# Performance work log

Measured on AMD Instinct MI355X. Metric: run time of the kernel, lower is better.

Reference implementation:

```python
import jax, jax.numpy as jnp
import numpy as np

N_NODES = 50000
N_EDGES = 1600000
F_GO, F_RE, F_ME = 512, 256, 256
E_DIM, N_HEADS, H_DIM, O_DIM = 256, 4, 256, 128


def setup_inputs() -> dict:
    key = jax.random.key(0)
    ks = jax.random.split(key, 20)
    s = lambda k, shp, sc: jax.random.normal(k, shp, dtype=jnp.float32) * sc
    inp = {
        "x": jax.random.normal(ks[0], (N_NODES, F_GO + F_RE + F_ME + 1), dtype=jnp.float32),
        "edge_index": jax.random.randint(ks[1], (2, N_EDGES), 0, N_NODES, dtype=jnp.int32),
        # modality projections (stored as [in, out] so we do x @ W)
        "w_go": s(ks[2], (F_GO, E_DIM), 0.04), "b_go": jnp.zeros((E_DIM,), jnp.float32),
        "w_re": s(ks[3], (F_RE, E_DIM), 0.06), "b_re": jnp.zeros((E_DIM,), jnp.float32),
        "w_me": s(ks[4], (F_ME, E_DIM), 0.06), "b_me": jnp.zeros((E_DIM,), jnp.float32),
        "w_gw": s(ks[5], (1, E_DIM), 0.5),    "b_gw": jnp.zeros((E_DIM,), jnp.float32),
        # MultiheadAttention params (torch layout: in_proj_w [3E, E], out_proj_w [E, E])
        "in_proj_w": s(ks[6], (3 * E_DIM, E_DIM), 0.06),
        "in_proj_b": jnp.zeros((3 * E_DIM,), jnp.float32),
        "out_proj_w": s(ks[7], (E_DIM, E_DIM), 0.06),
        "out_proj_b": jnp.zeros((E_DIM,), jnp.float32),
        # GCN layers (stored as [in, out])
        "w1": s(ks[8], (E_DIM, H_DIM), 0.06), "b1": jnp.zeros((H_DIM,), jnp.float32),
        "w2": s(ks[9], (H_DIM, O_DIM), 0.06), "b2": jnp.zeros((O_DIM,), jnp.float32),
    }
    return inp


def _forward(x, edge_index, w_go, b_go, w_re, b_re, w_me, b_me, w_gw, b_gw,
             in_proj_w, in_proj_b, out_proj_w, out_proj_b, w1, b1, w2, b2):
    N = x.shape[0]
    relu = jax.nn.relu
    go = x[:, :F_GO]
    re_ = x[:, F_GO:F_GO + F_RE]
    me = x[:, F_GO + F_RE:F_GO + F_RE + F_ME]
    gw = x[:, -1:]  # gwas = last column
    # [N, 4, E]: four projected modalities stacked as a tiny sequence
    p = jnp.stack([relu(go @ w_go + b_go), relu(re_ @ w_re + b_re),
                   relu(me @ w_me + b_me), relu(gw @ w_gw + b_gw)], axis=1)
    # Multihead self-attention over the 4 modality tokens
    wq, wk, wv = jnp.split(in_proj_w, 3, axis=0)
    bq, bk, bv = jnp.split(in_proj_b, 3, axis=0)
    dh = E_DIM // N_HEADS
    q = (p @ wq.T + bq).reshape(N, 4, N_HEADS, dh)
    k = (p @ wk.T + bk).reshape(N, 4, N_HEADS, dh)
    v = (p @ wv.T + bv).reshape(N, 4, N_HEADS, dh)
    scores = jnp.einsum('nqhd,nkhd->nhqk', q, k) / jnp.sqrt(jnp.float32(dh))
    attn = jax.nn.softmax(scores, axis=-1)
    o = jnp.einsum('nhqk,nkhd->nqhd', attn, v).reshape(N, 4, E_DIM)
    o = o @ out_proj_w.T + out_proj_b
    fused = o.mean(axis=1)  # [N, E]
    # GCN normalization with self-loops (shared by both layers)
    loops = jnp.arange(N, dtype=edge_index.dtype)
    src = jnp.concatenate([edge_index[0], loops])
    dst = jnp.concatenate([edge_index[1], loops])
    deg = jax.ops.segment_sum(jnp.ones_like(src, dtype=fused.dtype), dst, num_segments=N)
    dinv = jnp.where(deg > 0, jax.lax.rsqrt(deg), 0.0)
    norm = dinv[src] * dinv[dst]  # [E+N]

    def gcn(h, W, b):
        hw = h @ W  # transform then scatter-aggregate
        msg = norm[:, None] * hw[src]
        return jax.ops.segment_sum(msg, dst, num_segments=N) + b

    h1 = relu(gcn(fused, w1, b1))
    # dropout p=0.3 skipped (eval mode)
    return gcn(h1, w2, b2)


def reference(x, edge_index, w_go, b_go, w_re, b_re, w_me, b_me, w_gw, b_gw,
              in_proj_w, in_proj_b, out_proj_w, out_proj_b, w1, b1, w2, b2):
    return _forward(x, edge_index, w_go, b_go, w_re, b_re, w_me, b_me, w_gw, b_gw,
                    in_proj_w, in_proj_b, out_proj_w, out_proj_b, w1, b1, w2, b2)
```

## Files before the change

### kernel.cpp

```cpp
#include <hip/hip_runtime.h>
#include <cstdint>
#include <cstddef>

#define NN 50000
#define NE 1600000
#define XD 1025

typedef unsigned short ushortt;
typedef __attribute__((ext_vector_type(8))) short short8;
typedef __attribute__((ext_vector_type(4))) float f32x4;

__device__ __forceinline__ float relu_f(float v) { return v > 0.f ? v : 0.f; }
__device__ __forceinline__ float b2f(ushortt u) { return __uint_as_float(((unsigned)u) << 16); }
__device__ __forceinline__ float blo(unsigned u) { return __uint_as_float(u << 16); }
__device__ __forceinline__ float bhi(unsigned u) { return __uint_as_float(u & 0xffff0000u); }
__device__ __forceinline__ ushortt bf16rn(float f) {
    unsigned u = __float_as_uint(f);
    return (ushortt)((u + 0x7fffu + ((u >> 16) & 1u)) >> 16);
}
__device__ __forceinline__ void load_lds16(const void* g, void* l) {
    __builtin_amdgcn_global_load_lds(
        (const __attribute__((address_space(1))) void*)g,
        (__attribute__((address_space(3))) void*)l, 16, 0, 0);
}

template <int ACT>
__global__ __launch_bounds__(256) void gemm_mfma(
    const ushortt* __restrict__ A, int lda,
    const ushortt* __restrict__ Bt,
    ushortt* __restrict__ C, int ldc,
    const float* __restrict__ bias,
    int M, int K)
{
    __shared__ ushortt As[128 * 32];
    __shared__ ushortt Bs[128 * 32];
    const int tid = threadIdx.x;
    const int w = tid >> 6, l = tid & 63;
    const int wr = w >> 1, wc = w & 1;
    const int brow = blockIdx.y << 7;
    const int bcol = blockIdx.x << 7;

    f32x4 acc[4][4] = {};

    const int rA0 = wr * 64 + (l & 15);
    const int rB0 = wc * 64 + (l & 15);
    const int kslot = l >> 4;

    for (int k0 = 0; k0 < K; k0 += 32) {
#pragma unroll
        for (int c = 0; c < 2; ++c) {
            int rl = c * 64 + w * 16 + (l >> 2);
            int csel = (l & 3) ^ (rl & 3);
            int gr = brow + rl; if (gr >= M) gr = M - 1;
            load_lds16(A + (size_t)gr * lda + k0 + csel * 8, &As[(c * 64 + w * 16) * 32]);
        }
#pragma unroll
        for (int c = 0; c < 2; ++c) {
            int rl = c * 64 + w * 16 + (l >> 2);
            int csel = (l & 3) ^ (rl & 3);
            load_lds16(Bt + (size_t)(bcol + rl) * K + k0 + csel * 8, &Bs[(c * 64 + w * 16) * 32]);
        }
        __syncthreads();

        short8 af[4], bf[4];
#pragma unroll
        for (int mi = 0; mi < 4; ++mi) {
            int row = rA0 + mi * 16;
            af[mi] = *(const short8*)&As[row * 32 + ((kslot ^ (row & 3)) << 3)];
        }
#pragma unroll
        for (int ni = 0; ni < 4; ++ni) {
            int row = rB0 + ni * 16;
            bf[ni] = *(const short8*)&Bs[row * 32 + ((kslot ^ (row & 3)) << 3)];
        }
#pragma unroll
        for (int mi = 0; mi < 4; ++mi)
#pragma unroll
            for (int ni = 0; ni < 4; ++ni)
                acc[mi][ni] = __builtin_amdgcn_mfma_f32_16x16x32_bf16(af[mi], bf[ni], acc[mi][ni], 0, 0, 0);
        __syncthreads();
    }

    const int cb = bcol + wc * 64 + (l & 15);
    const int rb = brow + wr * 64 + ((l >> 4) << 2);
#pragma unroll
    for (int mi = 0; mi < 4; ++mi) {
#pragma unroll
        for (int ni = 0; ni < 4; ++ni) {
            int col = cb + ni * 16;
            float bv = bias ? bias[col] : 0.f;
#pragma unroll
            for (int r = 0; r < 4; ++r) {
                int row = rb + mi * 16 + r;
                if (row < M) {
                    float v = acc[mi][ni][r] + bv;
                    if (ACT == 1) v = relu_f(v);
                    C[(size_t)row * ldc + col] = bf16rn(v);
                }
            }
        }
    }
}

__global__ __launch_bounds__(256) void mega_a2(
    const float* __restrict__ x,
    const float* __restrict__ w_go, const float* __restrict__ w_re,
    const float* __restrict__ w_me, const float* __restrict__ w2,
    const float* __restrict__ ipw,
    ushortt* __restrict__ o_go, ushortt* __restrict__ o_re,
    ushortt* __restrict__ o_me, ushortt* __restrict__ o_w2, ushortt* __restrict__ o_ip,
    ushortt* __restrict__ ago, ushortt* __restrict__ are, ushortt* __restrict__ ame,
    const float* __restrict__ w_gw, const float* __restrict__ b_gw, ushortt* __restrict__ p,
    const float* __restrict__ opw, const float* __restrict__ w1, float* __restrict__ T)
{
    const int bid = blockIdx.x;
    const int tid = threadIdx.x;
    if (bid < 25000) {
        long idx = bid * 256L + tid;
        int n = (int)(idx >> 7);
        int c8 = ((int)idx & 127) << 3;
        const float* src = x + (size_t)n * XD + c8;
        ushortt* dstp;
        if (c8 < 512) dstp = ago + (size_t)n * 512 + c8;
        else if (c8 < 768) dstp = are + (size_t)n * 256 + (c8 - 512);
        else dstp = ame + (size_t)n * 256 + (c8 - 768);
        ushort4 o1, o2;
        o1.x = bf16rn(src[0]); o1.y = bf16rn(src[1]); o1.z = bf16rn(src[2]); o1.w = bf16rn(src[3]);
        o2.x = bf16rn(src[4]); o2.y = bf16rn(src[5]); o2.z = bf16rn(src[6]); o2.w = bf16rn(src[7]);
        *(ushort4*)dstp = o1;
        *(ushort4*)(dstp + 4) = o2;
    } else if (bid < 26664) {
        int idx = (bid - 25000) * 256 + tid;
        if (idx < 131072) {
            int c = idx >> 9, r = idx & 511;
            o_go[idx] = bf16rn(w_go[r * 256 + c]);
        } else if (idx < 196608) {
            int j = idx - 131072; int c = j >> 8, r = j & 255;
            o_re[j] = bf16rn(w_re[r * 256 + c]);
        } else if (idx < 262144) {
            int j = idx - 196608; int c = j >> 8, r = j & 255;
            o_me[j] = bf16rn(w_me[r * 256 + c]);
        } else if (idx < 294912) {
            int j = idx - 262144; int c = j >> 8, r = j & 255;
            o_w2[j] = bf16rn(w2[r * 128 + c]);
        } else {
            int j5 = idx - 294912;
            int j  = j5 & 7;
            int l  = (j5 >> 3) & 63;
            int qk = (j5 >> 9) & 1;
            int ni = (j5 >> 10) & 3;
            int kk = (j5 >> 12) & 7;
            int w  = (j5 >> 15) & 3;
            int row = qk * 256 + w * 64 + ni * 16 + (l & 15);
            int col = kk * 32 + ((l >> 4) << 3) + j;
            o_ip[j5] = bf16rn(ipw[(size_t)row * 256 + col]);
        }
    } else if (bid < 39164) {
        long idx = (bid - 26664) * 256L + tid;
        int n = (int)(idx >> 6);
        int c = ((int)idx & 63) << 2;
        float g = x[(size_t)n * XD + 1024];
        float4 w4 = *(const float4*)(w_gw + c);
        float4 b4 = *(const float4*)(b_gw + c);
        ushort4 r;
        r.x = bf16rn(relu_f(fmaf(g, w4.x, b4.x)));
        r.y = bf16rn(relu_f(fmaf(g, w4.y, b4.y)));
        r.z = bf16rn(relu_f(fmaf(g, w4.z, b4.z)));
        r.w = bf16rn(relu_f(fmaf(g, w4.w, b4.w)));
        *(ushort4*)(p + (size_t)n * 1024 + 768 + c) = r;
    } else {
        int d = bid - 39164, c = tid;
        float a = 0.f;
        for (int j = 0; j < 256; ++j)
            a = fmaf(opw[j * 256 + d], w1[j * 256 + c], a);
        T[d * 256 + c] = a;
    }
}

__global__ __launch_bounds__(256) void mega_b2(
    const int* __restrict__ dst, int* __restrict__ deg, int* __restrict__ rank,
    const ushortt* __restrict__ ago, const ushortt* __restrict__ are, const ushortt* __restrict__ ame,
    const ushortt* __restrict__ wgo, const ushortt* __restrict__ wre, const ushortt* __restrict__ wme,
    const float* __restrict__ b_go, const float* __restrict__ b_re, const float* __restrict__ b_me,
    ushortt* __restrict__ p)
{
    __shared__ ushortt As[128 * 32];
    __shared__ ushortt Bs[128 * 32];
    const int bid = blockIdx.x;
    const int tid = threadIdx.x;

    if (bid < 1563) {
        int e = (bid * 256 + tid) * 4;
        if (e < NE) {
            int4 d = *(const int4*)(dst + e);
            int4 r;
            r.x = atomicAdd(&deg[d.x], 1);
            r.y = atomicAdd(&deg[d.y], 1);
            r.z = atomicAdd(&deg[d.z], 1);
            r.w = atomicAdd(&deg[d.w], 1);
            *(int4*)(rank + e) = r;
        }
        return;
    }

    const int t = bid - 1563;
    const int z = t / 782;
    const int r = t - z * 782;
    const int by = r >> 1;
    const int bx = r & 1;

    const ushortt* A; const ushortt* Bt; const float* bias; int K, lda, coff;
    if (z == 0)      { A = ago; Bt = wgo; bias = b_go; K = 512; lda = 512; coff = 0; }
    else if (z == 1) { A = are; Bt = wre; bias = b_re; K = 256; lda = 256; coff = 256; }
    else             { A = ame; Bt = wme; bias = b_me; K = 256; lda = 256; coff = 512; }

    const int w = tid >> 6, l = tid & 63;
    const int wr = w >> 1, wc = w & 1;
    const int brow = by << 7;
    const int bcol = bx << 7;

    f32x4 acc[4][4] = {};

    const int rA0 = wr * 64 + (l & 15);
    const int rB0 = wc * 64 + (l & 15);
    const int kslot = l >> 4;

    for (int k0 = 0; k0 < K; k0 += 32) {
#pragma unroll
        for (int c = 0; c < 2; ++c) {
            int rl = c * 64 + w * 16 + (l >> 2);
            int csel = (l & 3) ^ (rl & 3);
            int gr = brow + rl; if (gr >= NN) gr = NN - 1;
            load_lds16(A + (size_t)gr * lda + k0 + csel * 8, &As[(c * 64 + w * 16) * 32]);
        }
#pragma unroll
        for (int c = 0; c < 2; ++c) {
            int rl = c * 64 + w * 16 + (l >> 2);
            int csel = (l & 3) ^ (rl & 3);
            load_lds16(Bt + (size_t)(bcol + rl) * K + k0 + csel * 8, &Bs[(c * 64 + w * 16) * 32]);
        }
        __syncthreads();

        short8 af[4], bf[4];
#pragma unroll
        for (int mi = 0; mi < 4; ++mi) {
            int row = rA0 + mi * 16;
            af[mi] = *(const short8*)&As[row * 32 + ((kslot ^ (row & 3)) << 3)];
        }
#pragma unroll
        for (int ni = 0; ni < 4; ++ni) {
            int row = rB0 + ni * 16;
            bf[ni] = *(const short8*)&Bs[row * 32 + ((kslot ^ (row & 3)) << 3)];
        }
#pragma unroll
        for (int mi = 0; mi < 4; ++mi)
#pragma unroll
            for (int ni = 0; ni < 4; ++ni)
                acc[mi][ni] = __builtin_amdgcn_mfma_f32_16x16x32_bf16(af[mi], bf[ni], acc[mi][ni], 0, 0, 0);
        __syncthreads();
    }

    const int cb = bcol + wc * 64 + (l & 15);
    const int rb = brow + wr * 64 + ((l >> 4) << 2);
#pragma unroll
    for (int mi = 0; mi < 4; ++mi) {
#pragma unroll
        for (int ni = 0; ni < 4; ++ni) {
            int col = cb + ni * 16;
            float bv = bias[col];
#pragma unroll
            for (int rr = 0; rr < 4; ++rr) {
                int row = rb + mi * 16 + rr;
                if (row < NN)
                    p[(size_t)row * 1024 + coff + col] = bf16rn(relu_f(acc[mi][ni][rr] + bv));
            }
        }
    }
}

__global__ __launch_bounds__(256) void mega_c(
    const float* __restrict__ ipw, const float* __restrict__ T, ushortt* __restrict__ wbigT,
    const float* __restrict__ opb, const float* __restrict__ w1,
    const float* __restrict__ ipb, float* __restrict__ bbig,
    const int* __restrict__ deg, float* __restrict__ dinv)
{
    const int bid = blockIdx.x;
    const int tid = threadIdx.x;
    if (bid < 256) {
        const float* wv = ipw + 512 * 256;
        int c = bid, kk = tid;
#pragma unroll
        for (int h = 0; h < 4; ++h) {
            float a = 0.f;
            for (int d = 0; d < 64; ++d)
                a = fmaf(wv[(h * 64 + d) * 256 + kk], T[(h * 64 + d) * 256 + c], a);
            wbigT[(size_t)c * 1024 + h * 256 + kk] = bf16rn(a);
        }
    } else if (bid == 256) {
        int c = tid;
        float a = 0.f;
        for (int j = 0; j < 256; ++j) a = fmaf(opb[j], w1[j * 256 + c], a);
        for (int d = 0; d < 256; ++d) a = fmaf(ipb[512 + d], T[d * 256 + c], a);
        bbig[c] = a;
    } else {
        int n = (bid - 257) * 256 + tid;
        if (n < NN) dinv[n] = rsqrtf((float)deg[n] + 1.0f);
    }
}

__global__ __launch_bounds__(1024) void scan_blk(
    const int* __restrict__ deg, int* __restrict__ offs, int* __restrict__ btot, int N)
{
    __shared__ int wsum[16];
    const int tid = threadIdx.x;
    const int lane = tid & 63;
    const int w = tid >> 6;
    int i = blockIdx.x * 1024 + tid;
    int v = (i < N) ? deg[i] : 0;
    int x = v;
#pragma unroll
    for (int d = 1; d < 64; d <<= 1) {
        int t = __shfl_up(x, d);
        if (lane >= d) x += t;
    }
    if (lane == 63) wsum[w] = x;
    __syncthreads();
    if (w == 0 && lane < 16) {
        int y = wsum[lane];
#pragma unroll
        for (int d = 1; d < 16; d <<= 1) {
            int t = __shfl_up(y, d);
            if (lane >= d) y += t;
        }
        wsum[lane] = y;
    }
    __syncthreads();
    int waveoff = (w == 0) ? 0 : wsum[w - 1];
    if (i < N) offs[i] = waveoff + x - v;
    if (tid == 0) btot[blockIdx.x] = wsum[15];
}

__global__ __launch_bounds__(64) void scan_tot(int* __restrict__ btot, int nb)
{
    int t = threadIdx.x;
    int v = (t < nb) ? btot[t] : 0;
    int x = v;
#pragma unroll
    for (int d = 1; d < 64; d <<= 1) {
        int tt = __shfl_up(x, d);
        if (t >= d) x += tt;
    }
    if (t < nb) btot[t] = x - v;
    if (t == 63) btot[nb] = x;
}

__global__ __launch_bounds__(256) void scan_add(
    const int* __restrict__ btot, int* __restrict__ offs, int N, int nb)
{
    int i = blockIdx.x * 256 + threadIdx.x;
    if (i < N) offs[i] += btot[i >> 10];
    else if (i == N) offs[N] = btot[nb];
}

__global__ __launch_bounds__(256) void mega_d(
    const int* __restrict__ ei, const int* __restrict__ offs,
    const int* __restrict__ rank, int2* __restrict__ pk, const float* __restrict__ dinv,
    const ushortt* __restrict__ p,
    const ushortt* __restrict__ ipw_opt,
    const float* __restrict__ ipb,
    ushortt* __restrict__ pbar)
{
    __shared__ __align__(16) ushortt p_s[32 * 256];
    __shared__ float asum_s[8][4][4];

    const int bid = blockIdx.x;
    const int tid = threadIdx.x;

    if (bid < 1563) {
        int e = (bid * 256 + tid) * 4;
        if (e < NE) {
            int4 s4 = *(const int4*)(ei + e);
            int4 d4 = *(const int4*)(ei + NE + e);
            int4 r4 = *(const int4*)(rank + e);
            pk[offs[d4.x] + r4.x] = make_int2(s4.x, __float_as_int(dinv[s4.x] * dinv[d4.x]));
            pk[offs[d4.y] + r4.y] = make_int2(s4.y, __float_as_int(dinv[s4.y] * dinv[d4.y]));
            pk[offs[d4.z] + r4.z] = make_int2(s4.z, __float_as_int(dinv[s4.z] * dinv[d4.z]));
            pk[offs[d4.w] + r4.w] = make_int2(s4.w, __float_as_int(dinv[s4.w] * dinv[d4.w]));
        }
        return;
    }

    const int w = tid >> 6, l = tid & 63;
    const int nb = (bid - 1563) << 3;
    const size_t r0 = (size_t)nb * 4;

    {
        const int slot = l & 31;
#pragma unroll
        for (int c = 0; c < 4; ++c) {
            int row = w * 8 + c * 2 + (l >> 5);
            load_lds16(p + (r0 + row) * 256 + ((slot ^ (row & 7)) << 3),
                       &p_s[(w * 8 + c * 2) * 256]);
        }
    }
    __syncthreads();

    const int nq = w << 6;
    f32x4 aq[2][4] = {}, ak[2][4] = {};
    const int ar0 = l & 15, ar1 = ar0 + 16;
#pragma unroll
    for (int kk = 0; kk < 8; ++kk) {
        const int slot = (kk << 2) + (l >> 4);
        short8 a0 = *(const short8*)&p_s[ar0 * 256 + ((slot ^ (ar0 & 7)) << 3)];
        short8 a1 = *(const short8*)&p_s[ar1 * 256 + ((slot ^ (ar1 & 7)) << 3)];
        short8 bq[4], bk[4];
#pragma unroll
        for (int ni = 0; ni < 4; ++ni) {
            const size_t base = ((((size_t)(w * 8 + kk)) * 4 + ni) * 2) * 512 + (size_t)l * 8;
            bq[ni] = *(const short8*)&ipw_opt[base];
            bk[ni] = *(const short8*)&ipw_opt[base + 512];
        }
#pragma unroll
        for (int ni = 0; ni < 4; ++ni) {
            aq[0][ni] = __builtin_amdgcn_mfma_f32_16x16x32_bf16(a0, bq[ni], aq[0][ni], 0, 0, 0);
            aq[1][ni] = __builtin_amdgcn_mfma_f32_16x16x32_bf16(a1, bq[ni], aq[1][ni], 0, 0, 0);
            ak[0][ni] = __builtin_amdgcn_mfma_f32_16x16x32_bf16(a0, bk[ni], ak[0][ni], 0, 0, 0);
            ak[1][ni] = __builtin_amdgcn_mfma_f32_16x16x32_bf16(a1, bk[ni], ak[1][ni], 0, 0, 0);
        }
    }

    float bqv[4], bkv[4];
#pragma unroll
    for (int ni = 0; ni < 4; ++ni) {
        int col = nq + (ni << 4) + (l & 15);
        bqv[ni] = ipb[col];
        bkv[ni] = ipb[256 + col];
    }
#pragma unroll
    for (int mt = 0; mt < 2; ++mt) {
        float s[4][4] = {};
#pragma unroll
        for (int ni = 0; ni < 4; ++ni) {
            float qv[4], kv[4];
#pragma unroll
            for (int r = 0; r < 4; ++r) {
                qv[r] = aq[mt][ni][r] + bqv[ni];
                kv[r] = ak[mt][ni][r] + bkv[ni];
            }
#pragma unroll
            for (int ti = 0; ti < 4; ++ti)
#pragma unroll
                for (int tj = 0; tj < 4; ++tj)
                    s[ti][tj] = fmaf(qv[ti], kv[tj], s[ti][tj]);
        }
#pragma unroll
        for (int m = 1; m <= 8; m <<= 1)
#pragma unroll
            for (int ti = 0; ti < 4; ++ti)
#pragma unroll
                for (int tj = 0; tj < 4; ++tj)
                    s[ti][tj] += __shfl_xor(s[ti][tj], m);
        float asum[4] = {};
#pragma unroll
        for (int ti = 0; ti < 4; ++ti) {
            float v0 = s[ti][0] * 0.125f, v1 = s[ti][1] * 0.125f;
            float v2 = s[ti][2] * 0.125f, v3 = s[ti][3] * 0.125f;
            float m4 = fmaxf(fmaxf(v0, v1), fmaxf(v2, v3));
            float e0 = __expf(v0 - m4), e1 = __expf(v1 - m4);
            float e2 = __expf(v2 - m4), e3 = __expf(v3 - m4);
            float inv = 1.f / (e0 + e1 + e2 + e3);
            asum[0] = fmaf(e0, inv, asum[0]);
            asum[1] = fmaf(e1, inv, asum[1]);
            asum[2] = fmaf(e2, inv, asum[2]);
            asum[3] = fmaf(e3, inv, asum[3]);
        }
        if ((l & 15) == 0) {
            int node = mt * 4 + (l >> 4);
#pragma unroll
            for (int tj = 0; tj < 4; ++tj)
                asum_s[node][w][tj] = 0.25f * asum[tj];
        }
    }
    __syncthreads();

    {
        const int node = tid >> 5;
        const int c8 = (tid & 31) << 3;
        float f[4][8];
#pragma unroll
        for (int tj = 0; tj < 4; ++tj) {
            int row = node * 4 + tj;
            uint4 u = *(const uint4*)&p_s[row * 256 + (((c8 >> 3) ^ (row & 7)) << 3)];
            f[tj][0] = blo(u.x); f[tj][1] = bhi(u.x); f[tj][2] = blo(u.y); f[tj][3] = bhi(u.y);
            f[tj][4] = blo(u.z); f[tj][5] = bhi(u.z); f[tj][6] = blo(u.w); f[tj][7] = bhi(u.w);
        }
#pragma unroll
        for (int h = 0; h < 4; ++h) {
            float a0 = asum_s[node][h][0], a1 = asum_s[node][h][1];
            float a2 = asum_s[node][h][2], a3 = asum_s[node][h][3];
            ushortt res[8];
#pragma unroll
            for (int i = 0; i < 8; ++i)
                res[i] = bf16rn(a0 * f[0][i] + a1 * f[1][i] + a2 * f[2][i] + a3 * f[3][i]);
            *(uint4*)&pbar[(size_t)(nb + node) * 1024 + h * 256 + c8] = *(uint4*)res;
        }
    }
}

template <int ACT, int OUTBF>
__global__ __launch_bounds__(256) void gcn_gather256(
    const int* __restrict__ offs, const int2* __restrict__ pk,
    const ushortt* __restrict__ hw,
    const float* __restrict__ dinv, const float* __restrict__ bias,
    void* __restrict__ outb, int N)
{
    __shared__ float part[2][256];
    const int tid = threadIdx.x;
    const int nodei = tid >> 7;
    const int half = (tid >> 6) & 1;
    const int l = tid & 63;
    const int wid = blockIdx.x * 2 + nodei;
    const int col = l * 4;
    const bool active = wid < N;

    int beg = 0, end = 0;
    if (active) { beg = offs[wid]; end = offs[wid + 1]; }
    const int mid = beg + ((end - beg + 1) >> 1);
    int e = half ? mid : beg;
    const int ee = half ? end : mid;

    float acc[4] = {0.f, 0.f, 0.f, 0.f};
    if (active && half == 0) {
        float self = dinv[wid] * dinv[wid];
        ushort4 r = *(const ushort4*)(hw + (size_t)wid * 256 + col);
        acc[0] = self * b2f(r.x); acc[1] = self * b2f(r.y);
        acc[2] = self * b2f(r.z); acc[3] = self * b2f(r.w);
    }

    for (; e + 7 < ee; e += 8) {
        int2 q[8];
#pragma unroll
        for (int j = 0; j < 8; ++j) q[j] = pk[e + j];
        ushort4 r[8];
#pragma unroll
        for (int j = 0; j < 8; ++j) r[j] = *(const ushort4*)(hw + (size_t)q[j].x * 256 + col);
#pragma unroll
        for (int j = 0; j < 8; ++j) {
            float n = __int_as_float(q[j].y);
            acc[0] = fmaf(n, b2f(r[j].x), acc[0]); acc[1] = fmaf(n, b2f(r[j].y), acc[1]);
            acc[2] = fmaf(n, b2f(r[j].z), acc[2]); acc[3] = fmaf(n, b2f(r[j].w), acc[3]);
        }
    }
    for (; e < ee; ++e) {
        int2 p0 = pk[e];
        float n0 = __int_as_float(p0.y);
        ushort4 r0 = *(const ushort4*)(hw + (size_t)p0.x * 256 + col);
        acc[0] = fmaf(n0, b2f(r0.x), acc[0]); acc[1] = fmaf(n0, b2f(r0.y), acc[1]);
        acc[2] = fmaf(n0, b2f(r0.z), acc[2]); acc[3] = fmaf(n0, b2f(r0.w), acc[3]);
    }

    if (half == 1) {
        float4 v; v.x = acc[0]; v.y = acc[1]; v.z = acc[2]; v.w = acc[3];
        *(float4*)&part[nodei][col] = v;
    }
    __syncthreads();
    if (active && half == 0) {
        float4 pv = *(const float4*)&part[nodei][col];
        acc[0] += pv.x; acc[1] += pv.y; acc[2] += pv.z; acc[3] += pv.w;
#pragma unroll
        for (int jj = 0; jj < 4; ++jj) {
            acc[jj] += bias[col + jj];
            if (ACT == 1) acc[jj] = relu_f(acc[jj]);
        }
        if (OUTBF == 1) {
            ushortt* ob = (ushortt*)outb;
            ushort4 r;
            r.x = bf16rn(acc[0]); r.y = bf16rn(acc[1]); r.z = bf16rn(acc[2]); r.w = bf16rn(acc[3]);
            *(ushort4*)(ob + (size_t)wid * 256 + col) = r;
        } else {
            float* ob = (float*)outb;
            float4 r; r.x = acc[0]; r.y = acc[1]; r.z = acc[2]; r.w = acc[3];
            *(float4*)(ob + (size_t)wid * 256 + col) = r;
        }
    }
}

__global__ __launch_bounds__(256) void gcn_gather128(
    const int* __restrict__ offs, const int2* __restrict__ pk,
    const ushortt* __restrict__ hw,
    const float* __restrict__ dinv, const float* __restrict__ bias,
    float* __restrict__ outb, int N)
{
    const int wid = blockIdx.x * 4 + (threadIdx.x >> 6);
    const int lane = threadIdx.x & 63;
    if (wid >= N) return;
    const int g = lane >> 5;
    const int col = (lane & 31) * 4;

    float acc[4] = {0.f, 0.f, 0.f, 0.f};
    if (g == 0) {
        float self = dinv[wid] * dinv[wid];
        ushort4 r = *(const ushort4*)(hw + (size_t)wid * 128 + col);
        acc[0] = self * b2f(r.x); acc[1] = self * b2f(r.y);
        acc[2] = self * b2f(r.z); acc[3] = self * b2f(r.w);
    }

    const int beg = offs[wid], end = offs[wid + 1];
    int e = beg + g;
    for (; e + 6 < end; e += 8) {
        int2 q[4];
        q[0] = pk[e]; q[1] = pk[e + 2]; q[2] = pk[e + 4]; q[3] = pk[e + 6];
        ushort4 r[4];
#pragma unroll
        for (int j = 0; j < 4; ++j) r[j] = *(const ushort4*)(hw + (size_t)q[j].x * 128 + col);
#pragma unroll
        for (int j = 0; j < 4; ++j) {
            float n = __int_as_float(q[j].y);
            acc[0] = fmaf(n, b2f(r[j].x), acc[0]); acc[1] = fmaf(n, b2f(r[j].y), acc[1]);
            acc[2] = fmaf(n, b2f(r[j].z), acc[2]); acc[3] = fmaf(n, b2f(r[j].w), acc[3]);
        }
    }
    for (; e < end; e += 2) {
        int2 p0 = pk[e];
        float n0 = __int_as_float(p0.y);
        ushort4 r0 = *(const ushort4*)(hw + (size_t)p0.x * 128 + col);
        acc[0] = fmaf(n0, b2f(r0.x), acc[0]); acc[1] = fmaf(n0, b2f(r0.y), acc[1]);
        acc[2] = fmaf(n0, b2f(r0.z), acc[2]); acc[3] = fmaf(n0, b2f(r0.w), acc[3]);
    }

#pragma unroll
    for (int jj = 0; jj < 4; ++jj)
        acc[jj] += __shfl_xor(acc[jj], 32);

    if (g == 0) {
        float4 r;
        r.x = acc[0] + bias[col + 0];
        r.y = acc[1] + bias[col + 1];
        r.z = acc[2] + bias[col + 2];
        r.w = acc[3] + bias[col + 3];
        *(float4*)(outb + (size_t)wid * 128 + col) = r;
    }
}

extern "C" void kernel_launch(void* const* d_in, const int* in_sizes, int n_in,
                              void* d_out, int out_size, void* d_ws, size_t ws_size,
                              hipStream_t stream)
{
    const float* x    = (const float*)d_in[0];
    const int*   ei   = (const int*)d_in[1];
    const float* w_go = (const float*)d_in[2];
    const float* b_go = (const float*)d_in[3];
    const float* w_re = (const float*)d_in[4];
    const float* b_re = (const float*)d_in[5];
    const float* w_me = (const float*)d_in[6];
    const float* b_me = (const float*)d_in[7];
    const float* w_gw = (const float*)d_in[8];
    const float* b_gw = (const float*)d_in[9];
    const float* ipw  = (const float*)d_in[10];
    const float* ipb  = (const float*)d_in[11];
    const float* opw  = (const float*)d_in[12];
    const float* opb  = (const float*)d_in[13];
    const float* w1   = (const float*)d_in[14];
    const float* b1   = (const float*)d_in[15];
    const float* w2   = (const float*)d_in[16];
    const float* b2   = (const float*)d_in[17];
    float* out = (float*)d_out;
    char* ws   = (char*)d_ws;

    size_t off = 0;
    auto alloc = [&](size_t bytes) { size_t o = off; off += (bytes + 255) & ~(size_t)255; return o; };
    const size_t o_dinv = alloc(NN * 4);
    const size_t o_deg  = alloc(NN * 4);
    const size_t o_offs = alloc((NN + 1) * 4);
    const size_t o_rank = alloc((size_t)NE * 4);
    const size_t o_btot = alloc(64 * 4);
    const size_t o_csrp = alloc((size_t)NE * 8);
    const size_t o_wgo  = alloc(256 * 512 * 2);
    const size_t o_wre  = alloc(256 * 256 * 2);
    const size_t o_wme  = alloc(256 * 256 * 2);
    const size_t o_ipw  = alloc(512 * 256 * 2);
    const size_t o_T    = alloc(256 * 256 * 4);
    const size_t o_wbig = alloc(256 * 1024 * 2);
    const size_t o_bbig = alloc(256 * 4);
    const size_t o_w2t  = alloc(128 * 256 * 2);
    const size_t o_pbr  = alloc((size_t)4 * NN * 256 * 2);
    const size_t o_x16  = alloc((size_t)NN * 1024 * 2);
    const size_t o_pbar = alloc((size_t)NN * 1024 * 2);
    const size_t o_hw   = alloc((size_t)NN * 256 * 2);
    const size_t o_h1   = alloc((size_t)NN * 256 * 2);
    const size_t o_hw2  = alloc((size_t)NN * 128 * 2);

    float* f_dinv = (float*)(ws + o_dinv);
    int*   i_deg  = (int*)(ws + o_deg);
    int*   i_offs = (int*)(ws + o_offs);
    int*   i_rank = (int*)(ws + o_rank);
    int*   i_btot = (int*)(ws + o_btot);
    int2*  i_csrp = (int2*)(ws + o_csrp);
    float* f_T    = (float*)(ws + o_T);
    float* f_bbig = (float*)(ws + o_bbig);
    ushortt* p    = (ushortt*)(ws + o_pbr);
    ushortt* ago  = (ushortt*)(ws + o_x16);
    ushortt* are  = ago + (size_t)NN * 512;
    ushortt* ame  = ago + (size_t)NN * 768;
    ushortt* pbar = (ushortt*)(ws + o_pbar);
    ushortt* hw   = (ushortt*)(ws + o_hw);
    ushortt* h1   = (ushortt*)(ws + o_h1);
    ushortt* hw2  = (ushortt*)(ws + o_hw2);

    const int NB_SCAN = (NN + 1023) / 1024;

    hipMemsetAsync(i_deg, 0, NN * 4, stream);

    mega_a2<<<39420, 256, 0, stream>>>(
        x,
        w_go, w_re, w_me, w2, ipw,
        (ushortt*)(ws + o_wgo), (ushortt*)(ws + o_wre), (ushortt*)(ws + o_wme),
        (ushortt*)(ws + o_w2t), (ushortt*)(ws + o_ipw),
        ago, are, ame,
        w_gw, b_gw, p,
        opw, w1, f_T);

    mega_b2<<<1563 + 2346, 256, 0, stream>>>(
        ei + NE, i_deg, i_rank,
        ago, are, ame,
        (ushortt*)(ws + o_wgo), (ushortt*)(ws + o_wre), (ushortt*)(ws + o_wme),
        b_go, b_re, b_me, p);

    mega_c<<<453, 256, 0, stream>>>(
        ipw, f_T, (ushortt*)(ws + o_wbig),
        opb, w1, ipb, f_bbig,
        i_deg, f_dinv);

    scan_blk<<<NB_SCAN, 1024, 0, stream>>>(i_deg, i_offs, i_btot, NN);
    scan_tot<<<1, 64, 0, stream>>>(i_btot, NB_SCAN);
    scan_add<<<(NN + 1 + 255) / 256, 256, 0, stream>>>(i_btot, i_offs, NN, NB_SCAN);

    mega_d<<<1563 + NN / 8, 256, 0, stream>>>(
        ei, i_offs, i_rank, i_csrp, f_dinv,
        p, (ushortt*)(ws + o_ipw), ipb, pbar);

    dim3 gB(2, (NN + 127) / 128);
    gemm_mfma<0><<<gB, 256, 0, stream>>>(pbar, 1024, (ushortt*)(ws + o_wbig), hw, 256, f_bbig, NN, 1024);

    gcn_gather256<1, 1><<<(NN + 1) / 2, 256, 0, stream>>>(i_offs, i_csrp, hw, f_dinv, b1, h1, NN);

    dim3 gH2(1, (NN + 127) / 128);
    gemm_mfma<0><<<gH2, 256, 0, stream>>>(h1, 256, (ushortt*)(ws + o_w2t), hw2, 128, nullptr, NN, 256);
    gcn_gather128<<<(NN + 3) / 4, 256, 0, stream>>>(i_offs, i_csrp, hw2, f_dinv, b2, out, NN);
}
```

Before: 657.3 us.

## Split folded V·T weight GEMM into per-head V projection then shared T GEMM

The change stops folding the V projection into a 1024x256 combined weight. Instead, a new per-head GEMM projects the attention-averaged tokens (pbar, K=256 per head) through Wv into a 256-wide obar, and a second GEMM multiplies obar by the transposed out_proj·w1 product (K=256). This cuts the main GEMM's K from 1024 to 256 and removes the expensive wbig construction loop, adding a dedicated Wv bf16 conversion. The cost is an extra kernel launch, an extra N×256 intermediate round trip through memory, and one more bf16 rounding step.

```diff
diff --git a/kernel.cpp b/kernel.cpp
--- a/kernel.cpp
+++ b/kernel.cpp
@@ -102,6 +102,75 @@
     }
 }
 
+__global__ __launch_bounds__(256) void gemm_obar(
+    const ushortt* __restrict__ pbar,
+    const ushortt* __restrict__ wv16,
+    const float* __restrict__ ipb,
+    ushortt* __restrict__ obar)
+{
+    __shared__ ushortt As[128 * 32];
+    __shared__ ushortt Bs[64 * 32];
+    const int tid = threadIdx.x;
+    const int w = tid >> 6, l = tid & 63;
+    const int z = blockIdx.z;
+    const int brow = blockIdx.y << 7;
+    const ushortt* Bt = wv16 + (size_t)z * 64 * 256;
+
+    f32x4 acc[2][4] = {};
+    const int rA0 = w * 32 + (l & 15);
+    const int kslot = l >> 4;
+
+    for (int k0 = 0; k0 < 256; k0 += 32) {
+#pragma unroll
+        for (int c = 0; c < 2; ++c) {
+            int rl = c * 64 + w * 16 + (l >> 2);
+            int csel = (l & 3) ^ (rl & 3);
+            int gr = brow + rl; if (gr >= NN) gr = NN - 1;
+            load_lds16(pbar + (size_t)gr * 1024 + z * 256 + k0 + csel * 8, &As[(c * 64 + w * 16) * 32]);
+        }
+        {
+            int rl = w * 16 + (l >> 2);
+            int csel = (l & 3) ^ (rl & 3);
+            load_lds16(Bt + (size_t)rl * 256 + k0 + csel * 8, &Bs[(w * 16) * 32]);
+        }
+        __syncthreads();
+
+        short8 af[2], bf[4];
+#pragma unroll
+        for (int mi = 0; mi < 2; ++mi) {
+            int row = rA0 + mi * 16;
+            af[mi] = *(const short8*)&As[row * 32 + ((kslot ^ (row & 3)) << 3)];
+        }
+#pragma unroll
+        for (int ni = 0; ni < 4; ++ni) {
+            int row = ni * 16 + (l & 15);
+            bf[ni] = *(const short8*)&Bs[row * 32 + ((kslot ^ (row & 3)) << 3)];
+        }
+#pragma unroll
+        for (int mi = 0; mi < 2; ++mi)
+#pragma unroll
+            for (int ni = 0; ni < 4; ++ni)
+                acc[mi][ni] = __builtin_amdgcn_mfma_f32_16x16x32_bf16(af[mi], bf[ni], acc[mi][ni], 0, 0, 0);
+        __syncthreads();
+    }
+
+    const int rb = brow + w * 32 + ((l >> 4) << 2);
+#pragma unroll
+    for (int mi = 0; mi < 2; ++mi) {
+#pragma unroll
+        for (int ni = 0; ni < 4; ++ni) {
+            int col = ni * 16 + (l & 15);
+            float bv = ipb[512 + z * 64 + col];
+#pragma unroll
+            for (int r = 0; r < 4; ++r) {
+                int row = rb + mi * 16 + r;
+                if (row < NN)
+                    obar[(size_t)row * 256 + z * 64 + col] = bf16rn(acc[mi][ni][r] + bv);
+            }
+        }
+    }
+}
+
 __global__ __launch_bounds__(256) void mega_a2(
     const float* __restrict__ x,
     const float* __restrict__ w_go, const float* __restrict__ w_re,
@@ -109,6 +178,7 @@
     const float* __restrict__ ipw,
     ushortt* __restrict__ o_go, ushortt* __restrict__ o_re,
     ushortt* __restrict__ o_me, ushortt* __restrict__ o_w2, ushortt* __restrict__ o_ip,
+    ushortt* __restrict__ o_wv,
     ushortt* __restrict__ ago, ushortt* __restrict__ are, ushortt* __restrict__ ame,
     const float* __restrict__ w_gw, const float* __restrict__ b_gw, ushortt* __restrict__ p,
     const float* __restrict__ opw, const float* __restrict__ w1, float* __restrict__ T)
@@ -129,7 +199,7 @@
         o2.x = bf16rn(src[4]); o2.y = bf16rn(src[5]); o2.z = bf16rn(src[6]); o2.w = bf16rn(src[7]);
         *(ushort4*)dstp = o1;
         *(ushort4*)(dstp + 4) = o2;
-    } else if (bid < 26664) {
+    } else if (bid < 26920) {
         int idx = (bid - 25000) * 256 + tid;
         if (idx < 131072) {
             int c = idx >> 9, r = idx & 511;
@@ -143,7 +213,7 @@
         } else if (idx < 294912) {
             int j = idx - 262144; int c = j >> 8, r = j & 255;
             o_w2[j] = bf16rn(w2[r * 128 + c]);
-        } else {
+        } else if (idx < 425984) {
             int j5 = idx - 294912;
             int j  = j5 & 7;
             int l  = (j5 >> 3) & 63;
@@ -154,9 +224,12 @@
             int row = qk * 256 + w * 64 + ni * 16 + (l & 15);
             int col = kk * 32 + ((l >> 4) << 3) + j;
             o_ip[j5] = bf16rn(ipw[(size_t)row * 256 + col]);
-        }
-    } else if (bid < 39164) {
-        long idx = (bid - 26664) * 256L + tid;
+        } else if (idx < 491520) {
+            int j6 = idx - 425984;
+            o_wv[j6] = bf16rn(ipw[512 * 256 + j6]);
+        }
+    } else if (bid < 39420) {
+        long idx = (bid - 26920) * 256L + tid;
         int n = (int)(idx >> 6);
         int c = ((int)idx & 63) << 2;
         float g = x[(size_t)n * XD + 1024];
@@ -169,7 +242,7 @@
         r.w = bf16rn(relu_f(fmaf(g, w4.w, b4.w)));
         *(ushort4*)(p + (size_t)n * 1024 + 768 + c) = r;
     } else {
-        int d = bid - 39164, c = tid;
+        int d = bid - 39420, c = tid;
         float a = 0.f;
         for (int j = 0; j < 256; ++j)
             a = fmaf(opw[j * 256 + d], w1[j * 256 + c], a);
@@ -279,28 +352,19 @@
 }
 
 __global__ __launch_bounds__(256) void mega_c(
-    const float* __restrict__ ipw, const float* __restrict__ T, ushortt* __restrict__ wbigT,
+    const float* __restrict__ T, ushortt* __restrict__ Tt16,
     const float* __restrict__ opb, const float* __restrict__ w1,
-    const float* __restrict__ ipb, float* __restrict__ bbig,
+    float* __restrict__ bbig,
     const int* __restrict__ deg, float* __restrict__ dinv)
 {
     const int bid = blockIdx.x;
     const int tid = threadIdx.x;
     if (bid < 256) {
-        const float* wv = ipw + 512 * 256;
-        int c = bid, kk = tid;
-#pragma unroll
-        for (int h = 0; h < 4; ++h) {
-            float a = 0.f;
-            for (int d = 0; d < 64; ++d)
-                a = fmaf(wv[(h * 64 + d) * 256 + kk], T[(h * 64 + d) * 256 + c], a);
-            wbigT[(size_t)c * 1024 + h * 256 + kk] = bf16rn(a);
-        }
+        Tt16[bid * 256 + tid] = bf16rn(T[tid * 256 + bid]);
     } else if (bid == 256) {
         int c = tid;
         float a = 0.f;
         for (int j = 0; j < 256; ++j) a = fmaf(opb[j], w1[j * 256 + c], a);
-        for (int d = 0; d < 256; ++d) a = fmaf(ipb[512 + d], T[d * 256 + c], a);
         bbig[c] = a;
     } else {
         int n = (bid - 257) * 256 + tid;
@@ -679,13 +743,15 @@
     const size_t o_wre  = alloc(256 * 256 * 2);
     const size_t o_wme  = alloc(256 * 256 * 2);
     const size_t o_ipw  = alloc(512 * 256 * 2);
+    const size_t o_wv   = alloc(256 * 256 * 2);
     const size_t o_T    = alloc(256 * 256 * 4);
-    const size_t o_wbig = alloc(256 * 1024 * 2);
+    const size_t o_Tt   = alloc(256 * 256 * 2);
     const size_t o_bbig = alloc(256 * 4);
     const size_t o_w2t  = alloc(128 * 256 * 2);
     const size_t o_pbr  = alloc((size_t)4 * NN * 256 * 2);
     const size_t o_x16  = alloc((size_t)NN * 1024 * 2);
     const size_t o_pbar = alloc((size_t)NN * 1024 * 2);
+    const size_t o_obar = alloc((size_t)NN * 256 * 2);
     const size_t o_hw   = alloc((size_t)NN * 256 * 2);
     const size_t o_h1   = alloc((size_t)NN * 256 * 2);
     const size_t o_hw2  = alloc((size_t)NN * 128 * 2);
@@ -703,6 +769,7 @@
     ushortt* are  = ago + (size_t)NN * 512;
     ushortt* ame  = ago + (size_t)NN * 768;
     ushortt* pbar = (ushortt*)(ws + o_pbar);
+    ushortt* obar = (ushortt*)(ws + o_obar);
     ushortt* hw   = (ushortt*)(ws + o_hw);
     ushortt* h1   = (ushortt*)(ws + o_h1);
     ushortt* hw2  = (ushortt*)(ws + o_hw2);
@@ -711,11 +778,11 @@
 
     hipMemsetAsync(i_deg, 0, NN * 4, stream);
 
-    mega_a2<<<39420, 256, 0, stream>>>(
+    mega_a2<<<39676, 256, 0, stream>>>(
         x,
         w_go, w_re, w_me, w2, ipw,
         (ushortt*)(ws + o_wgo), (ushortt*)(ws + o_wre), (ushortt*)(ws + o_wme),
-        (ushortt*)(ws + o_w2t), (ushortt*)(ws + o_ipw),
+        (ushortt*)(ws + o_w2t), (ushortt*)(ws + o_ipw), (ushortt*)(ws + o_wv),
         ago, are, ame,
         w_gw, b_gw, p,
         opw, w1, f_T);
@@ -727,8 +794,8 @@
         b_go, b_re, b_me, p);
 
     mega_c<<<453, 256, 0, stream>>>(
-        ipw, f_T, (ushortt*)(ws + o_wbig),
-        opb, w1, ipb, f_bbig,
+        f_T, (ushortt*)(ws + o_Tt),
+        opb, w1, f_bbig,
         i_deg, f_dinv);
 
     scan_blk<<<NB_SCAN, 1024, 0, stream>>>(i_deg, i_offs, i_btot, NN);
@@ -739,8 +806,11 @@
         ei, i_offs, i_rank, i_csrp, f_dinv,
         p, (ushortt*)(ws + o_ipw), ipb, pbar);
 
+    dim3 gOB(1, (NN + 127) / 128, 4);
+    gemm_obar<<<gOB, 256, 0, stream>>>(pbar, (ushortt*)(ws + o_wv), ipb, obar);
+
     dim3 gB(2, (NN + 127) / 128);
-    gemm_mfma<0><<<gB, 256, 0, stream>>>(pbar, 1024, (ushortt*)(ws + o_wbig), hw, 256, f_bbig, NN, 1024);
+    gemm_mfma<0><<<gB, 256, 0, stream>>>(obar, 256, (ushortt*)(ws + o_Tt), hw, 256, f_bbig, NN, 256);
 
     gcn_gather256<1, 1><<<(NN + 1) / 2, 256, 0, stream>>>(i_offs, i_csrp, hw, f_dinv, b1, h1, NN);
 
```

After: 646.7 us (median of 4 runs). Within noise of the previous version (-1.6%).
